# Kernel optimization log

Measured on AMD Instinct MI355X. Metric: run time of the kernel, lower is better.

Reference implementation:

```python
import jax, jax.numpy as jnp
import numpy as np

# Constructor constants (init_kwargs)
DX = 10.0        # grid spacing [m]
DT = 0.001       # time step [s]
PML_FREQ = 15.0  # dominant frequency (used only for PML design in deepwave; see notes)
PML = 35         # pml_width
HALF = 4         # half-width of 8th-order stencil
NY, NX = 100, 200
NT = 300
N_SHOTS, N_SRC, N_REC = 2, 1, 100

# 8th-order central second-derivative coefficients, offsets -4..4
C2 = np.array([-1/560, 8/315, -1/5, 8/5, -205/72, 8/5, -1/5, 8/315, -1/560], np.float32)
# 8th-order central first-derivative coefficients, offsets -4..4
C1 = np.array([1/280, -4/105, 1/5, -4/5, 0.0, 4/5, -1/5, 4/105, -1/280], np.float32)


def shift_sum(u, coefs, axis):
    """Apply a 9-tap 1D stencil along `axis` (zero boundary outside the padded grid)."""
    pad = [(0, 0)] * u.ndim
    pad[axis] = (HALF, HALF)
    up = jnp.pad(u, pad)
    n = u.shape[axis]
    acc = jnp.zeros_like(u)
    for k in range(2 * HALF + 1):
        sl = [slice(None)] * u.ndim
        sl[axis] = slice(k, k + n)
        acc = acc + coefs[k] * up[tuple(sl)]
    return acc


def _sigma(n, vmax):
    # Quadratic PML damping profile, sigma_max from R=1e-3 reflection coefficient.
    d = jnp.arange(n, dtype=jnp.float32)
    r = jnp.maximum(jnp.maximum((PML - d) / PML, (d - (n - 1 - PML)) / PML), 0.0)
    smax = 3.0 * vmax * np.float32(np.log(1000.0)) / (2.0 * PML * DX)
    return smax * r * r


def _propagate(vp, src, src_loc, rec_loc):
    S, _, nt = src.shape
    v = jnp.pad(vp, PML, mode="edge")          # [ny, nx] padded grid
    ny, nx = v.shape
    v2 = (v * v)[None]                           # [1, ny, nx]
    vmax = jnp.max(vp)
    sy = _sigma(ny, vmax)
    sx = _sigma(nx, vmax)
    s = (sy[:, None] + sx[None, :])[None]        # combined damping
    pr = (sy[:, None] * sx[None, :])[None]       # corner cross term
    by = jnp.exp(-sy * DT)[None, :, None]        # CPML recursion factors
    bx = jnp.exp(-sx * DT)[None, None, :]
    c2 = jnp.asarray(C2) / np.float32(DX * DX)
    c1 = jnp.asarray(C1) / np.float32(DX)
    sids = jnp.arange(S)[:, None]
    syi = src_loc[..., 0] + PML
    sxi = src_loc[..., 1] + PML
    ryi = rec_loc[..., 0] + PML
    rxi = rec_loc[..., 1] + PML
    dt2 = np.float32(DT * DT)

    def step(carry, f_t):
        u, um, py, px = carry
        # CPML memory variables for the first derivatives
        py = by * py + (by - 1.0) * shift_sum(u, c1, 1)
        px = bx * px + (bx - 1.0) * shift_sum(u, c1, 2)
        lap = (shift_sum(u, c2, 1) + shift_sum(u, c2, 2)
               + shift_sum(py, c1, 1) + shift_sum(px, c1, 2))
        f = jnp.zeros_like(u).at[sids, syi, sxi].add(f_t)
        un = ((2.0 - pr * dt2) * u - (1.0 - 0.5 * s * DT) * um
              + dt2 * v2 * (lap + f)) / (1.0 + 0.5 * s * DT)
        rec = un[sids, ryi, rxi]                 # [S, n_rec]
        return (un, u, py, px), rec

    z = jnp.zeros((S, ny, nx), vp.dtype)
    xs = jnp.moveaxis(src, -1, 0)                # [nt, S, n_src]
    _, recs = jax.lax.scan(jax.checkpoint(step), (z, z, z, z), xs)
    return jnp.moveaxis(recs, 0, -1)             # [S, n_rec, nt]


def setup_inputs() -> dict:
    key = jax.random.key(0)
    k1, k2, k3, k4 = jax.random.split(key, 4)
    vp = 1500.0 + 2500.0 * jax.random.uniform(k1, (NY, NX), jnp.float32)
    src = jax.random.normal(k2, (N_SHOTS, N_SRC, NT), jnp.float32)
    src_loc = jax.random.randint(k3, (N_SHOTS, N_SRC, 2), 0, 90)
    rec_loc = jax.random.randint(k4, (N_SHOTS, N_REC, 2), 0, 90)
    return {"vp": vp, "src": src, "src_loc": src_loc, "rec_loc": rec_loc}


def reference(vp, src, src_loc, rec_loc):
    vx = _propagate(vp, src, src_loc, rec_loc)   # [S, n_rec, nt]
    # wrapper: vx.permute(0, 2, 1).unsqueeze(0) -> [1, S, nt, n_rec]
    return jnp.transpose(vx, (0, 2, 1))[None]
```

## Files before the change

kernel.cpp:

```cpp
#include <hip/hip_runtime.h>

constexpr int NY = 100, NX = 200;
constexpr int PML = 35;
constexpr int NYP = 170, NXP = 270;
constexpr int S = 2, NREC = 100, NT = 300;
constexpr float DX = 10.0f, DT = 1e-3f, DT2 = DT * DT;

constexpr int NTY = 16, NTX = 8;
constexpr int TY = 11, TX = 34;
constexpr int NBLKS = S * NTY * NTX;
constexpr int THREADS = 768;

constexpr int UW = 66;
constexpr int UH = TY + 16;
constexpr int PYH = TY + 8;
constexpr int PXW = 66;
constexpr int BXW = TX + 8;

constexpr int CELLS_NS = 8 * TX;
constexpr int CELLS_WE = TY * 8;
constexpr int OFF_N = 0;
constexpr int OFF_S = CELLS_NS;
constexpr int OFF_W = 2 * CELLS_NS;
constexpr int OFF_E = 2 * CELLS_NS + CELLS_WE;
constexpr int STAGE_CELLS = 2 * CELLS_NS + 2 * CELLS_WE;

typedef unsigned long long u64;

__device__ __constant__ float C2D[9] = {
    (float)(-1.0/560.0/100.0), (float)(8.0/315.0/100.0), (float)(-1.0/5.0/100.0),
    (float)(8.0/5.0/100.0),    (float)(-205.0/72.0/100.0), (float)(8.0/5.0/100.0),
    (float)(-1.0/5.0/100.0),   (float)(8.0/315.0/100.0),  (float)(-1.0/560.0/100.0)};
__device__ __constant__ float C1D[9] = {
    (float)(1.0/280.0/10.0), (float)(-4.0/105.0/10.0), (float)(1.0/5.0/10.0),
    (float)(-4.0/5.0/10.0),  0.0f,                     (float)(4.0/5.0/10.0),
    (float)(-1.0/5.0/10.0),  (float)(4.0/105.0/10.0),  (float)(-1.0/280.0/10.0)};

__device__ __forceinline__ u64 gload64(const u64* p) {
    return __hip_atomic_load(p, __ATOMIC_RELAXED, __HIP_MEMORY_SCOPE_AGENT);
}
__device__ __forceinline__ void gstore64(u64* p, u64 v) {
    __hip_atomic_store(p, v, __ATOMIC_RELAXED, __HIP_MEMORY_SCOPE_AGENT);
}

__device__ __forceinline__ float sigma_of(int d, int n, float smax) {
    float r = fmaxf(fmaxf((float)(PML - d) / (float)PML,
                          (float)(d - (n - 1 - PML)) / (float)PML), 0.0f);
    return smax * r * r;
}

__global__ void vmax_kernel(const float* __restrict__ vp, float* __restrict__ cst) {
    __shared__ float red[256];
    float m = 0.0f;
    for (int i = threadIdx.x; i < NY * NX; i += 256) m = fmaxf(m, vp[i]);
    red[threadIdx.x] = m;
    __syncthreads();
    for (int s2 = 128; s2 > 0; s2 >>= 1) {
        if (threadIdx.x < s2) red[threadIdx.x] = fmaxf(red[threadIdx.x], red[threadIdx.x + s2]);
        __syncthreads();
    }
    if (threadIdx.x == 0)
        cst[0] = 3.0f * red[0] * logf(1000.0f) / (2.0f * PML * DX);
}

__global__ __launch_bounds__(THREADS) void persist_kernel(
    const float* __restrict__ vp, const float* __restrict__ src,
    const int* __restrict__ src_loc, const int* __restrict__ rec_loc,
    float* __restrict__ out, u64* __restrict__ stage,
    const float* __restrict__ cst) {

    __shared__ float uS[2][UH * UW];
    __shared__ float pyS[2][PYH * TX];
    __shared__ float pxS[2][TY * PXW];
    __shared__ float byS[PYH], bymS[PYH], bxS[BXW], bxmS[BXW];
    __shared__ float srcS[NT];

    const int tid = threadIdx.x;
    const int bid = blockIdx.x;
    const int sh  = bid / (NTY * NTX);
    const int tr  = bid - sh * (NTY * NTX);
    const int tyi = tr / NTX, txi = tr - tyi * NTX;
    const int y0 = tyi * TY, x0 = txi * TX;
    const int rows = min(TY, NYP - y0), cols = min(TX, NXP - x0);
    const float smax = cst[0];

    for (int i = tid; i < 2 * UH * UW; i += THREADS) ((float*)uS)[i] = 0.0f;
    for (int i = tid; i < 2 * PYH * TX; i += THREADS) ((float*)pyS)[i] = 0.0f;
    for (int i = tid; i < 2 * TY * PXW; i += THREADS) ((float*)pxS)[i] = 0.0f;

    if (tid < PYH) {
        int yy = y0 - 4 + tid;
        if (yy >= 0 && yy < NYP) {
            float b = __expf(-sigma_of(yy, NYP, smax) * DT);
            byS[tid] = b; bymS[tid] = b - 1.0f;
        } else { byS[tid] = 0.0f; bymS[tid] = 0.0f; }
    }
    if (tid < BXW) {
        int xx = x0 - 4 + tid;
        if (xx >= 0 && xx < NXP) {
            float b = __expf(-sigma_of(xx, NXP, smax) * DT);
            bxS[tid] = b; bxmS[tid] = b - 1.0f;
        } else { bxS[tid] = 0.0f; bxmS[tid] = 0.0f; }
    }

    const int role = tid & 1;
    const int cell = tid >> 1;
    const bool hasTask = (tid < 2 * rows * cols);
    const int y = hasTask ? cell / cols : 0;
    const int x = hasTask ? cell - y * cols : 0;

    float e_r = 0.0f, d_r = 0.0f, Av_r = 0.0f, Bv_r = 0.0f;
    if (hasTask && role == 0) {
        int gy = y0 + y, gx = x0 + x;
        int vy = min(max(gy - PML, 0), NY - 1), vx = min(max(gx - PML, 0), NX - 1);
        float v = vp[vy * NX + vx];
        e_r = DT2 * v * v;
        float syv = sigma_of(gy, NYP, smax), sxv = sigma_of(gx, NXP, smax);
        d_r  = 1.0f / (1.0f + 0.5f * (syv + sxv) * DT);
        Av_r = 2.0f - syv * sxv * DT2;
        Bv_r = 1.0f - 0.5f * (syv + sxv) * DT;
    }

    const int sy = src_loc[sh * 2 + 0] + PML, sx = src_loc[sh * 2 + 1] + PML;
    const bool ownSrc = (sy >= y0 && sy < y0 + rows && sx >= x0 && sx < x0 + cols);
    const bool isSrc = hasTask && (role == 0) && ownSrc &&
                       (y == sy - y0) && (x == sx - x0);
    if (ownSrc)
        for (int i = tid; i < NT; i += THREADS) srcS[i] = src[sh * NT + i];

    int recLds = -1, recOut = 0;
    if (tid < S * NREC) {
        int rs = tid / NREC, rr2 = tid - rs * NREC;
        int ry = rec_loc[(rs * NREC + rr2) * 2 + 0] + PML;
        int rx = rec_loc[(rs * NREC + rr2) * 2 + 1] + PML;
        if (rs == sh && ry >= y0 && ry < y0 + rows && rx >= x0 && rx < x0 + cols) {
            recLds = (ry - y0 + 8) * UW + (rx - x0 + 8);
            recOut = rs * NT * NREC + rr2;
        }
    }

    const int bN = (tyi > 0)       ? bid - NTX : -1;
    const int bS = (tyi < NTY - 1) ? bid + NTX : -1;
    const int bW = (txi > 0)       ? bid - 1   : -1;
    const int bE = (txi < NTX - 1) ? bid + 1   : -1;

    const int nNS = 8 * cols, nWE = rows * 8;
    const int nTot = 2 * nNS + 2 * nWE;

    int hLds = -1, hSrc = 0;
    if (tid < nTot) {
        int j = tid, nb = -1, o = 0, lds = -1;
        if (j < nNS) {
            nb = bN;
            int r2 = j / cols, c2 = j - r2 * cols;
            o = OFF_S + r2 * TX + c2;
            lds = r2 * UW + 8 + c2;
        } else if ((j -= nNS) < nNS) {
            nb = bS;
            int r2 = j / cols, c2 = j - r2 * cols;
            if (nb >= 0) {
                int rowsS = min(TY, NYP - (y0 + TY));
                if (r2 >= rowsS) nb = -1;
            }
            o = OFF_N + r2 * TX + c2;
            lds = (8 + rows + r2) * UW + 8 + c2;
        } else if ((j -= nNS) < nWE) {
            nb = bW;
            o = OFF_E + j;
            lds = (8 + (j >> 3)) * UW + (j & 7);
        } else {
            j -= nWE;
            nb = bE;
            o = OFF_W + j;
            lds = (8 + (j >> 3)) * UW + 8 + cols + (j & 7);
        }
        if (nb >= 0) { hLds = lds; hSrc = nb * 2 * STAGE_CELLS + o; }
    }
    const bool nv = (hLds >= 0);
    const u64* sA = stage + hSrc;

    int aN = -1, aS = -1, aW = -1, aE = -1;
    if (hasTask && role == 0) {
        if (y < 8)          aN = OFF_N + y * TX + x;
        if (y >= rows - 8)  aS = OFF_S + (y - (rows - 8)) * TX + x;
        if (x < 8)          aW = OFF_W + y * 8 + x;
        if (x >= cols - 8)  aE = OFF_E + y * 8 + (x - (cols - 8));
    }

    {
        const u64 PK0 = ((u64)1 << 32);
        u64* s0 = stage + (size_t)(bid * 2 + 0) * STAGE_CELLS;
        if (aN >= 0) gstore64(s0 + aN, PK0);
        if (aS >= 0) gstore64(s0 + aS, PK0);
        if (aW >= 0) gstore64(s0 + aW, PK0);
        if (aE >= 0) gstore64(s0 + aE, PK0);
    }
    __syncthreads();

    u64 pf = nv ? gload64(sA) : 0;

    float u_curr = 0.0f, u_prev = 0.0f;

    int pa = 0, pb = 0;
    for (int t = 0; t < NT; t++) {
        const int par = t & 1;
        float* uCur = uS[pa];
        float* uN   = uS[pa ^ 1];
        const float* pyO = pyS[pb];
        float*       pyN = pyS[pb ^ 1];
        const float* pxO = pxS[pb];
        float*       pxN = pxS[pb ^ 1];

        if (nv) {
            const int need = t + 1;
            const u64* sp = sA + (size_t)par * STAGE_CELLS;
            while ((int)(pf >> 32) < need) pf = gload64(sp);
            uCur[hLds] = __uint_as_float((unsigned)pf);
        }
        __syncthreads();

        if (t > 0 && recLds >= 0) out[recOut + (t - 1) * NREC] = uCur[recLds];

        u64* sb = stage + (size_t)(bid * 2 + (par ^ 1)) * STAGE_CELLS;
        if (hasTask) {
            const float* uBase = role ? &uCur[(8 + y) * UW + x]
                                      : &uCur[y * UW + 8 + x];
            const int uStr = role ? 1 : UW;
            const float* pBase = role ? &pxO[y * PXW + x] : &pyO[y * TX + x];
            const int pStr = role ? 1 : TX;
            const float* bb  = role ? &bxS[x]  : &byS[y];
            const float* bbm = role ? &bxmS[x] : &bymS[y];

            float up[17];
#pragma unroll
            for (int j = 0; j < 17; j++)
                up[j] = (j == 8) ? u_curr : uBase[j * uStr];

            float pn[9];
#pragma unroll
            for (int j = 0; j < 9; j++) {
                float d1a = 0.0f, d1b = 0.0f;
#pragma unroll
                for (int k = 0; k < 4; k++) {
                    d1a = fmaf(C1D[k],     up[j + k],     d1a);
                    d1b = fmaf(C1D[k + 5], up[j + k + 5], d1b);
                }
                pn[j] = fmaf(bb[j], pBase[j * pStr], bbm[j] * (d1a + d1b));
            }

            float d2 = 0.0f, d1p = 0.0f;
#pragma unroll
            for (int k = 0; k < 9; k++) {
                d2 = fmaf(C2D[k], up[4 + k], d2);
                if (k != 4) d1p = fmaf(C1D[k], pn[k], d1p);
            }
            const float partial = d2 + d1p;
            const float other = __shfl_xor(partial, 1);

            float unv = 0.0f;
            if (role == 0) {
                const float lap = partial + other;
                const float f = isSrc ? srcS[t] : 0.0f;
                unv = (Av_r * u_curr - Bv_r * u_prev + e_r * (lap + f)) * d_r;
                const u64 pk = ((u64)(unsigned)(t + 2) << 32) |
                               (u64)__float_as_uint(unv);
                if (aN >= 0) gstore64(sb + aN, pk);
                if (aS >= 0) gstore64(sb + aS, pk);
                if (aW >= 0) gstore64(sb + aW, pk);
                if (aE >= 0) gstore64(sb + aE, pk);
            }
            const float got = __shfl_xor(unv, 1);
            const float u_new = role ? got : unv;

            float* pDst = role ? pxN : pyN;
            pDst[role ? (y * PXW + x + 4) : ((y + 4) * TX + x)] = pn[4];
            const int lo = role ? x : y;
            const int hiLim = role ? cols : rows;
            if (lo < 4)
                pDst[role ? (y * PXW + x) : (y * TX + x)] = pn[0];
            if (lo >= hiLim - 4)
                pDst[role ? (y * PXW + x + 8) : ((y + 8) * TX + x)] = pn[8];

            if (role == 0) uN[(8 + y) * UW + 8 + x] = unv;
            u_prev = u_curr; u_curr = u_new;
        }

        if (nv) pf = gload64(sA + (size_t)(par ^ 1) * STAGE_CELLS);

        pa ^= 1; pb ^= 1;
    }

    __syncthreads();
    if (recLds >= 0) out[recOut + (NT - 1) * NREC] = uS[pa][recLds];
}

extern "C" void kernel_launch(void* const* d_in, const int* in_sizes, int n_in,
                              void* d_out, int out_size, void* d_ws, size_t ws_size,
                              hipStream_t stream) {
    const float* vp = (const float*)d_in[0];
    const float* src = (const float*)d_in[1];
    const int* src_loc = (const int*)d_in[2];
    const int* rec_loc = (const int*)d_in[3];
    float* out = (float*)d_out;

    float* ws = (float*)d_ws;
    float* cst = ws;
    u64* stage = (u64*)(ws + 32);

    hipMemsetAsync(d_ws, 0,
                   (size_t)32 * sizeof(float) +
                   (size_t)NBLKS * 2 * STAGE_CELLS * sizeof(u64),
                   stream);
    vmax_kernel<<<1, 256, 0, stream>>>(vp, cst);
    persist_kernel<<<NBLKS, THREADS, 0, stream>>>(
        vp, src, src_loc, rec_loc, out, stage, cst);
}
```

Measured before the change: 760.9 us.

## Split shared u field into transposed and row copies for unit-stride stencil reads

The single padded u tile in shared memory is replaced by two copies: one stored transposed, so the y-direction thread reads 17 consecutive words, and one stored row-major for the x-direction thread. Row strides are padded (35, 51, 19, 43) to reduce bank conflicts, and the p buffers follow the same layout. Each thread now writes its new u value into its own copy, and the previous u is read back from the destination buffer instead of being kept in registers. This removes the strided y-direction shared loads, at the cost of an extra shared read per step and a second shared copy of the u tile.

```diff
diff --git a/kernel.cpp b/kernel.cpp
--- a/kernel.cpp
+++ b/kernel.cpp
@@ -11,10 +11,15 @@
 constexpr int NBLKS = S * NTY * NTX;
 constexpr int THREADS = 768;
 
-constexpr int UW = 66;
-constexpr int UH = TY + 16;
-constexpr int PYH = TY + 8;
-constexpr int PXW = 66;
+constexpr int UTS = 35;
+constexpr int UTSZ = TX * UTS;
+constexpr int URS = 51;
+constexpr int URSZ = TY * URS;
+constexpr int PTS = 19;
+constexpr int PTSZ = TX * PTS;
+constexpr int PXS = 43;
+constexpr int PXSZ = TY * PXS;
+constexpr int BYW = TY + 8;
 constexpr int BXW = TX + 8;
 
 constexpr int CELLS_NS = 8 * TX;
@@ -69,10 +74,11 @@
     float* __restrict__ out, u64* __restrict__ stage,
     const float* __restrict__ cst) {
 
-    __shared__ float uS[2][UH * UW];
-    __shared__ float pyS[2][PYH * TX];
-    __shared__ float pxS[2][TY * PXW];
-    __shared__ float byS[PYH], bymS[PYH], bxS[BXW], bxmS[BXW];
+    __shared__ float uT[2][UTSZ];
+    __shared__ float uR[2][URSZ];
+    __shared__ float pyT[2][PTSZ];
+    __shared__ float pxR[2][PXSZ];
+    __shared__ float byS[BYW], bymS[BYW], bxS[BXW], bxmS[BXW];
     __shared__ float srcS[NT];
 
     const int tid = threadIdx.x;
@@ -84,11 +90,12 @@
     const int rows = min(TY, NYP - y0), cols = min(TX, NXP - x0);
     const float smax = cst[0];
 
-    for (int i = tid; i < 2 * UH * UW; i += THREADS) ((float*)uS)[i] = 0.0f;
-    for (int i = tid; i < 2 * PYH * TX; i += THREADS) ((float*)pyS)[i] = 0.0f;
-    for (int i = tid; i < 2 * TY * PXW; i += THREADS) ((float*)pxS)[i] = 0.0f;
-
-    if (tid < PYH) {
+    for (int i = tid; i < 2 * UTSZ; i += THREADS) ((float*)uT)[i] = 0.0f;
+    for (int i = tid; i < 2 * URSZ; i += THREADS) ((float*)uR)[i] = 0.0f;
+    for (int i = tid; i < 2 * PTSZ; i += THREADS) ((float*)pyT)[i] = 0.0f;
+    for (int i = tid; i < 2 * PXSZ; i += THREADS) ((float*)pxR)[i] = 0.0f;
+
+    if (tid < BYW) {
         int yy = y0 - 4 + tid;
         if (yy >= 0 && yy < NYP) {
             float b = __expf(-sigma_of(yy, NYP, smax) * DT);
@@ -134,7 +141,7 @@
         int ry = rec_loc[(rs * NREC + rr2) * 2 + 0] + PML;
         int rx = rec_loc[(rs * NREC + rr2) * 2 + 1] + PML;
         if (rs == sh && ry >= y0 && ry < y0 + rows && rx >= x0 && rx < x0 + cols) {
-            recLds = (ry - y0 + 8) * UW + (rx - x0 + 8);
+            recLds = (ry - y0) * URS + (rx - x0 + 8);
             recOut = rs * NT * NREC + rr2;
         }
     }
@@ -147,14 +154,14 @@
     const int nNS = 8 * cols, nWE = rows * 8;
     const int nTot = 2 * nNS + 2 * nWE;
 
-    int hLds = -1, hSrc = 0;
+    int hOff = -1, hSrc = 0, hTgt = 0;
     if (tid < nTot) {
-        int j = tid, nb = -1, o = 0, lds = -1;
+        int j = tid, nb = -1, o = 0, off = -1, tgt = 0;
         if (j < nNS) {
             nb = bN;
             int r2 = j / cols, c2 = j - r2 * cols;
             o = OFF_S + r2 * TX + c2;
-            lds = r2 * UW + 8 + c2;
+            off = c2 * UTS + r2; tgt = 0;
         } else if ((j -= nNS) < nNS) {
             nb = bS;
             int r2 = j / cols, c2 = j - r2 * cols;
@@ -163,20 +170,20 @@
                 if (r2 >= rowsS) nb = -1;
             }
             o = OFF_N + r2 * TX + c2;
-            lds = (8 + rows + r2) * UW + 8 + c2;
+            off = c2 * UTS + (8 + rows + r2); tgt = 0;
         } else if ((j -= nNS) < nWE) {
             nb = bW;
             o = OFF_E + j;
-            lds = (8 + (j >> 3)) * UW + (j & 7);
+            off = (j >> 3) * URS + (j & 7); tgt = 1;
         } else {
             j -= nWE;
             nb = bE;
             o = OFF_W + j;
-            lds = (8 + (j >> 3)) * UW + 8 + cols + (j & 7);
+            off = (j >> 3) * URS + 8 + cols + (j & 7); tgt = 1;
         }
-        if (nb >= 0) { hLds = lds; hSrc = nb * 2 * STAGE_CELLS + o; }
-    }
-    const bool nv = (hLds >= 0);
+        if (nb >= 0) { hOff = off; hTgt = tgt; hSrc = nb * 2 * STAGE_CELLS + o; }
+    }
+    const bool nv = (hOff >= 0);
     const u64* sA = stage + hSrc;
 
     int aN = -1, aS = -1, aW = -1, aE = -1;
@@ -199,42 +206,36 @@
 
     u64 pf = nv ? gload64(sA) : 0;
 
-    float u_curr = 0.0f, u_prev = 0.0f;
-
-    int pa = 0, pb = 0;
+    int pa = 0;
     for (int t = 0; t < NT; t++) {
         const int par = t & 1;
-        float* uCur = uS[pa];
-        float* uN   = uS[pa ^ 1];
-        const float* pyO = pyS[pb];
-        float*       pyN = pyS[pb ^ 1];
-        const float* pxO = pxS[pb];
-        float*       pxN = pxS[pb ^ 1];
+        float* uTc = uT[pa];       float* uRc = uR[pa];
+        float* uTn = uT[pa ^ 1];   float* uRn = uR[pa ^ 1];
+        const float* pyO = pyT[pa]; float* pyN = pyT[pa ^ 1];
+        const float* pxO = pxR[pa]; float* pxN = pxR[pa ^ 1];
 
         if (nv) {
             const int need = t + 1;
             const u64* sp = sA + (size_t)par * STAGE_CELLS;
             while ((int)(pf >> 32) < need) pf = gload64(sp);
-            uCur[hLds] = __uint_as_float((unsigned)pf);
+            (hTgt ? uRc : uTc)[hOff] = __uint_as_float((unsigned)pf);
         }
         __syncthreads();
 
-        if (t > 0 && recLds >= 0) out[recOut + (t - 1) * NREC] = uCur[recLds];
+        if (t > 0 && recLds >= 0) out[recOut + (t - 1) * NREC] = uRc[recLds];
 
         u64* sb = stage + (size_t)(bid * 2 + (par ^ 1)) * STAGE_CELLS;
         if (hasTask) {
-            const float* uBase = role ? &uCur[(8 + y) * UW + x]
-                                      : &uCur[y * UW + 8 + x];
-            const int uStr = role ? 1 : UW;
-            const float* pBase = role ? &pxO[y * PXW + x] : &pyO[y * TX + x];
-            const int pStr = role ? 1 : TX;
-            const float* bb  = role ? &bxS[x]  : &byS[y];
-            const float* bbm = role ? &bxmS[x] : &bymS[y];
+            const float* uSrc = role ? &uRc[y * URS + x] : &uTc[x * UTS + y];
+            const float* pSrc = role ? &pxO[y * PXS + x] : &pyO[x * PTS + y];
+            const float* bbp  = role ? &bxS[x]  : &byS[y];
+            const float* bbmp = role ? &bxmS[x] : &bymS[y];
+            float* pDst = role ? &pxN[y * PXS + x] : &pyN[x * PTS + y];
+            float* uDst = role ? &uRn[y * URS + x + 8] : &uTn[x * UTS + y + 8];
 
             float up[17];
 #pragma unroll
-            for (int j = 0; j < 17; j++)
-                up[j] = (j == 8) ? u_curr : uBase[j * uStr];
+            for (int j = 0; j < 17; j++) up[j] = uSrc[j];
 
             float pn[9];
 #pragma unroll
@@ -245,7 +246,7 @@
                     d1a = fmaf(C1D[k],     up[j + k],     d1a);
                     d1b = fmaf(C1D[k + 5], up[j + k + 5], d1b);
                 }
-                pn[j] = fmaf(bb[j], pBase[j * pStr], bbm[j] * (d1a + d1b));
+                pn[j] = fmaf(bbp[j], pSrc[j], bbmp[j] * (d1a + d1b));
             }
 
             float d2 = 0.0f, d1p = 0.0f;
@@ -257,11 +258,12 @@
             const float partial = d2 + d1p;
             const float other = __shfl_xor(partial, 1);
 
+            const float umv = uDst[0];
             float unv = 0.0f;
             if (role == 0) {
                 const float lap = partial + other;
                 const float f = isSrc ? srcS[t] : 0.0f;
-                unv = (Av_r * u_curr - Bv_r * u_prev + e_r * (lap + f)) * d_r;
+                unv = (Av_r * up[8] - Bv_r * umv + e_r * (lap + f)) * d_r;
                 const u64 pk = ((u64)(unsigned)(t + 2) << 32) |
                                (u64)__float_as_uint(unv);
                 if (aN >= 0) gstore64(sb + aN, pk);
@@ -270,28 +272,22 @@
                 if (aE >= 0) gstore64(sb + aE, pk);
             }
             const float got = __shfl_xor(unv, 1);
-            const float u_new = role ? got : unv;
-
-            float* pDst = role ? pxN : pyN;
-            pDst[role ? (y * PXW + x + 4) : ((y + 4) * TX + x)] = pn[4];
+            uDst[0] = role ? got : unv;
+
+            pDst[4] = pn[4];
             const int lo = role ? x : y;
             const int hiLim = role ? cols : rows;
-            if (lo < 4)
-                pDst[role ? (y * PXW + x) : (y * TX + x)] = pn[0];
-            if (lo >= hiLim - 4)
-                pDst[role ? (y * PXW + x + 8) : ((y + 8) * TX + x)] = pn[8];
-
-            if (role == 0) uN[(8 + y) * UW + 8 + x] = unv;
-            u_prev = u_curr; u_curr = u_new;
+            if (lo < 4)          pDst[0] = pn[0];
+            if (lo >= hiLim - 4) pDst[8] = pn[8];
         }
 
         if (nv) pf = gload64(sA + (size_t)(par ^ 1) * STAGE_CELLS);
 
-        pa ^= 1; pb ^= 1;
+        pa ^= 1;
     }
 
     __syncthreads();
-    if (recLds >= 0) out[recOut + (NT - 1) * NREC] = uS[pa][recLds];
+    if (recLds >= 0) out[recOut + (NT - 1) * NREC] = uR[pa][recLds];
 }
 
 extern "C" void kernel_launch(void* const* d_in, const int* in_sizes, int n_in,
```

New measurement: 830.4 us. 9.1% more time.

## Compute interior stencil before halo wait, finish halo contributions after

Applied to the files above, without the earlier changes.

Each step now adds an extra barrier, then computes the first-derivative and Laplacian contributions from tile-interior shared-memory values before spinning on the neighbour halo flags. After the halo arrives, only the halo-dependent terms are accumulated. This is meant to overlap stencil arithmetic with inter-block synchronization latency. The PML recursion factors are also hoisted into registers. The cost is higher register pressure, an extra __syncthreads per step, and more complex split accumulation.

```diff
diff --git a/kernel.cpp b/kernel.cpp
--- a/kernel.cpp
+++ b/kernel.cpp
@@ -15,6 +15,7 @@
 constexpr int UH = TY + 16;
 constexpr int PYH = TY + 8;
 constexpr int PXW = 66;
+constexpr int BYW = TY + 8;
 constexpr int BXW = TX + 8;
 
 constexpr int CELLS_NS = 8 * TX;
@@ -72,7 +73,7 @@
     __shared__ float uS[2][UH * UW];
     __shared__ float pyS[2][PYH * TX];
     __shared__ float pxS[2][TY * PXW];
-    __shared__ float byS[PYH], bymS[PYH], bxS[BXW], bxmS[BXW];
+    __shared__ float byS[BYW], bymS[BYW], bxS[BXW], bxmS[BXW];
     __shared__ float srcS[NT];
 
     const int tid = threadIdx.x;
@@ -88,7 +89,7 @@
     for (int i = tid; i < 2 * PYH * TX; i += THREADS) ((float*)pyS)[i] = 0.0f;
     for (int i = tid; i < 2 * TY * PXW; i += THREADS) ((float*)pxS)[i] = 0.0f;
 
-    if (tid < PYH) {
+    if (tid < BYW) {
         int yy = y0 - 4 + tid;
         if (yy >= 0 && yy < NYP) {
             float b = __expf(-sigma_of(yy, NYP, smax) * DT);
@@ -108,6 +109,8 @@
     const bool hasTask = (tid < 2 * rows * cols);
     const int y = hasTask ? cell / cols : 0;
     const int x = hasTask ? cell - y * cols : 0;
+    const int ivLo = role ? (8 - x) : (8 - y);
+    const int ivHi = role ? (7 + cols - x) : (7 + rows - y);
 
     float e_r = 0.0f, d_r = 0.0f, Av_r = 0.0f, Bv_r = 0.0f;
     if (hasTask && role == 0) {
@@ -197,19 +200,63 @@
     }
     __syncthreads();
 
+    float bbr[9], bbmr[9];
+#pragma unroll
+    for (int j = 0; j < 9; j++) {
+        bbr[j]  = hasTask ? (role ? bxS[x + j]  : byS[y + j])  : 0.0f;
+        bbmr[j] = hasTask ? (role ? bxmS[x + j] : bymS[y + j]) : 0.0f;
+    }
+
     u64 pf = nv ? gload64(sA) : 0;
 
     float u_curr = 0.0f, u_prev = 0.0f;
 
-    int pa = 0, pb = 0;
+    int pa = 0;
     for (int t = 0; t < NT; t++) {
         const int par = t & 1;
         float* uCur = uS[pa];
         float* uN   = uS[pa ^ 1];
-        const float* pyO = pyS[pb];
-        float*       pyN = pyS[pb ^ 1];
-        const float* pxO = pxS[pb];
-        float*       pxN = pxS[pb ^ 1];
+        const float* pyO = pyS[pa];
+        float*       pyN = pyS[pa ^ 1];
+        const float* pxO = pxS[pa];
+        float*       pxN = pxS[pa ^ 1];
+
+        __syncthreads();
+
+        if (t > 0 && recLds >= 0) out[recOut + (t - 1) * NREC] = uCur[recLds];
+
+        float pnS[9], pOv[9];
+        float d2S = 0.0f;
+        if (hasTask) {
+            const float* uSrc = role ? &uCur[(8 + y) * UW + x]
+                                     : &uCur[y * UW + 8 + x];
+            const int uStr = role ? 1 : UW;
+            const float* pSrc = role ? &pxO[y * PXW + x] : &pyO[y * TX + x];
+            const int pStr = role ? 1 : TX;
+
+            float up[17];
+            up[8] = u_curr;
+#pragma unroll
+            for (int j = 0; j < 17; j++) {
+                if (j == 8) continue;
+                up[j] = (j >= ivLo && j <= ivHi) ? uSrc[j * uStr] : 0.0f;
+            }
+#pragma unroll
+            for (int j = 0; j < 9; j++) pOv[j] = pSrc[j * pStr];
+
+#pragma unroll
+            for (int jj = 0; jj < 9; jj++) {
+                float a = 0.0f, b = 0.0f;
+#pragma unroll
+                for (int k = 0; k < 4; k++) {
+                    a = fmaf(C1D[k],     up[jj + k],     a);
+                    b = fmaf(C1D[k + 5], up[jj + k + 5], b);
+                }
+                pnS[jj] = a + b;
+            }
+#pragma unroll
+            for (int k = 0; k < 9; k++) d2S = fmaf(C2D[k], up[4 + k], d2S);
+        }
 
         if (nv) {
             const int need = t + 1;
@@ -219,42 +266,35 @@
         }
         __syncthreads();
 
-        if (t > 0 && recLds >= 0) out[recOut + (t - 1) * NREC] = uCur[recLds];
-
         u64* sb = stage + (size_t)(bid * 2 + (par ^ 1)) * STAGE_CELLS;
         if (hasTask) {
-            const float* uBase = role ? &uCur[(8 + y) * UW + x]
-                                      : &uCur[y * UW + 8 + x];
+            const float* uSrc = role ? &uCur[(8 + y) * UW + x]
+                                     : &uCur[y * UW + 8 + x];
             const int uStr = role ? 1 : UW;
-            const float* pBase = role ? &pxO[y * PXW + x] : &pyO[y * TX + x];
-            const int pStr = role ? 1 : TX;
-            const float* bb  = role ? &bxS[x]  : &byS[y];
-            const float* bbm = role ? &bxmS[x] : &bymS[y];
-
-            float up[17];
-#pragma unroll
-            for (int j = 0; j < 17; j++)
-                up[j] = (j == 8) ? u_curr : uBase[j * uStr];
-
+#pragma unroll
+            for (int j = 0; j < 17; j++) {
+                if (j == 8) continue;
+                if (j < ivLo || j > ivHi) {
+                    float h = uSrc[j * uStr];
+                    if (j >= 4 && j <= 12) d2S = fmaf(C2D[j - 4], h, d2S);
+#pragma unroll
+                    for (int jj = (j > 8 ? j - 8 : 0);
+                         jj <= (j < 8 ? j : 8); jj++) {
+                        if (jj == j - 4) continue;
+                        pnS[jj] = fmaf(C1D[j - jj], h, pnS[jj]);
+                    }
+                }
+            }
             float pn[9];
 #pragma unroll
-            for (int j = 0; j < 9; j++) {
-                float d1a = 0.0f, d1b = 0.0f;
-#pragma unroll
-                for (int k = 0; k < 4; k++) {
-                    d1a = fmaf(C1D[k],     up[j + k],     d1a);
-                    d1b = fmaf(C1D[k + 5], up[j + k + 5], d1b);
-                }
-                pn[j] = fmaf(bb[j], pBase[j * pStr], bbm[j] * (d1a + d1b));
-            }
-
-            float d2 = 0.0f, d1p = 0.0f;
-#pragma unroll
-            for (int k = 0; k < 9; k++) {
-                d2 = fmaf(C2D[k], up[4 + k], d2);
+            for (int j = 0; j < 9; j++)
+                pn[j] = fmaf(bbr[j], pOv[j], bbmr[j] * pnS[j]);
+            float d1p = 0.0f;
+#pragma unroll
+            for (int k = 0; k < 9; k++)
                 if (k != 4) d1p = fmaf(C1D[k], pn[k], d1p);
-            }
-            const float partial = d2 + d1p;
+
+            const float partial = d2S + d1p;
             const float other = __shfl_xor(partial, 1);
 
             float unv = 0.0f;
@@ -280,14 +320,13 @@
                 pDst[role ? (y * PXW + x) : (y * TX + x)] = pn[0];
             if (lo >= hiLim - 4)
                 pDst[role ? (y * PXW + x + 8) : ((y + 8) * TX + x)] = pn[8];
-
             if (role == 0) uN[(8 + y) * UW + 8 + x] = unv;
             u_prev = u_curr; u_curr = u_new;
         }
 
         if (nv) pf = gload64(sA + (size_t)(par ^ 1) * STAGE_CELLS);
 
-        pa ^= 1; pb ^= 1;
+        pa ^= 1;
     }
 
     __syncthreads();
```

New measurement: 1.132 ms. 48.7% more time.
